# Performance work log

Measured on AMD Instinct MI355X. Metric: run time of the kernel, lower is better.

## Reference

```python
import jax, jax.numpy as jnp
import numpy as np


def _make_pert(r, s):
    lin = np.linspace(-r, r, s)
    xm, ym, tm = np.meshgrid(lin, lin, lin)  # default 'xy' indexing, matches torch code
    return jnp.asarray(np.stack([xm.ravel(), ym.ravel(), tm.ravel()], axis=-1), dtype=jnp.float32)

PERTS = (_make_pert(0.01, 3), _make_pert(0.05, 5), _make_pert(0.09, 7))  # [27,3],[125,3],[343,3]

N, IN, H, HQ, FF, OUT = 4096, 3, 256, 64, 64, 3


def setup_inputs():
    key = jax.random.key(0)
    ks = jax.random.split(key, 24)

    def W(k, i, o):
        return (jax.random.normal(k, (i, o), jnp.float32) / np.sqrt(i)).astype(jnp.float32)

    one = jnp.ones((1,), jnp.float32)
    return {
        "x": jax.random.normal(ks[0], (N, 1), jnp.float32),
        "y": jax.random.normal(ks[1], (N, 1), jnp.float32),
        "t": jax.random.normal(ks[2], (N, 1), jnp.float32),
        # linear_emb: 3 -> 64 -> WaveAct -> 256
        "emb_W1": W(ks[3], IN, HQ), "emb_b1": jnp.zeros((HQ,), jnp.float32),
        "emb_wa": one, "emb_wb": one,
        "emb_W2": W(ks[4], HQ, H), "emb_b2": jnp.zeros((H,), jnp.float32),
        # multiregion_mixer: 4 -> 8 -> WaveAct -> 1
        "mix_W1": W(ks[5], 4, 8), "mix_b1": jnp.zeros((8,), jnp.float32),
        "mix_wa": one, "mix_wb": one,
        "mix_W2": W(ks[6], 8, 1), "mix_b2": jnp.zeros((1,), jnp.float32),
        "out_W0": W(ks[7], H, FF), "out_b0": jnp.zeros((FF,), jnp.float32),
        "out_wa0": one, "out_wb0": one,
        "out_Wh": jnp.stack([W(ks[8 + i], FF, FF) for i in range(3)]),
        "out_bh": jnp.zeros((3, FF), jnp.float32),
        "out_wah": jnp.ones((3, 1), jnp.float32), "out_wbh": jnp.ones((3, 1), jnp.float32),
        "out_Wf1": W(ks[11], FF, FF), "out_bf1": jnp.zeros((FF,), jnp.float32),
        "out_waf": one, "out_wbf": one,
        "out_Wf2": W(ks[12], FF, OUT), "out_bf2": jnp.zeros((OUT,), jnp.float32),
    }


def _wave(h, wa, wb):
    return wa * jnp.sin(h) + wb * jnp.cos(h)


def reference(x, y, t,
              emb_W1, emb_b1, emb_wa, emb_wb, emb_W2, emb_b2,
              mix_W1, mix_b1, mix_wa, mix_wb, mix_W2, mix_b2,
              out_W0, out_b0, out_wa0, out_wb0,
              out_Wh, out_bh, out_wah, out_wbh,
              out_Wf1, out_bf1, out_waf, out_wbf, out_Wf2, out_bf2):
    def emb(s):  # [..., 3] -> [..., 256]
        h = _wave(s @ emb_W1 + emb_b1, emb_wa, emb_wb)
        return h @ emb_W2 + emb_b2

    src = jnp.concatenate([x, y, t], axis=-1)           # [N, 3]
    feats = [emb(src)]                                   # region 1: unperturbed
    for P in PERTS:
        perturbed = src[:, None, :] + P[None, :, :]      # [N, P, 3]
        feats.append(emb(perturbed).mean(axis=1))        # [N, 256]
    stacked = jnp.stack(feats, axis=-1)                  # [N, 256, 4] (== permute(0,2,1) of stack dim=1)

    m = _wave(stacked @ mix_W1 + mix_b1, mix_wa, mix_wb) # [N, 256, 8]
    e = (m @ mix_W2 + mix_b2)[:, :, 0]                   # [N, 256]

    h = _wave(e @ out_W0 + out_b0, out_wa0, out_wb0)     # [N, 64]
    for i in range(3):                                   # fixed num_layer-1 = 3 hidden layers
        h = _wave(h @ out_Wh[i] + out_bh[i], out_wah[i], out_wbh[i])
    h = _wave(h @ out_Wf1 + out_bf1, out_waf, out_wbf)
    return h @ out_Wf2 + out_bf2                         # [N, 3]
```

## Files before the change

### kernel.cpp

```cpp
#include <hip/hip_runtime.h>

typedef _Float16 f16;
typedef _Float16 f16x8 __attribute__((ext_vector_type(8)));
typedef float v4f __attribute__((ext_vector_type(4)));

#define WS_W2T  0
#define WS_W0T  16384
#define WS_WHT  32768
#define WS_WF1T 45056
#define WS_CDW  24576

__global__ __launch_bounds__(256) void preprocess(
    const float* __restrict__ embW1, const float* __restrict__ embW2,
    const float* __restrict__ outW0, const float* __restrict__ outWh,
    const float* __restrict__ outWf1, f16* __restrict__ wsh)
{
    const int g = blockIdx.x * 256 + threadIdx.x;
    if (g < 16384) {
        const int c = g >> 6, k = g & 63;
        wsh[WS_W2T + g] = (f16)embW2[k*256 + c];
    } else if (g < 32768) {
        const int i = g - 16384;
        const int f = i >> 8, k = i & 255;
        wsh[WS_W0T + i] = (f16)outW0[k*64 + f];
    } else if (g < 45056) {
        const int i = g - 32768;
        const int l = i >> 12, f = (i >> 6) & 63, k = i & 63;
        wsh[WS_WHT + i] = (f16)outWh[l*4096 + k*64 + f];
    } else if (g < 49152) {
        const int i = g - 45056;
        const int f = i >> 6, k = i & 63;
        wsh[WS_WF1T + i] = (f16)outWf1[k*64 + f];
    } else if (g < 49344) {
        const int i = g - 49152;
        const int r = i >> 6, ch = i & 63;
        const float w0 = embW1[ch], w1 = embW1[64 + ch], w2 = embW1[128 + ch];
        float v;
        if (r == 0) {
            v = (1.f + 2.f*__cosf(0.01f*w0)) * (1.f + 2.f*__cosf(0.01f*w1))
              * (1.f + 2.f*__cosf(0.01f*w2)) * (1.f/27.f);
        } else if (r == 1) {
            v = (1.f + 2.f*(__cosf(0.025f*w0) + __cosf(0.05f*w0)))
              * (1.f + 2.f*(__cosf(0.025f*w1) + __cosf(0.05f*w1)))
              * (1.f + 2.f*(__cosf(0.025f*w2) + __cosf(0.05f*w2))) * (1.f/125.f);
        } else {
            v = (1.f + 2.f*(__cosf(0.03f*w0) + __cosf(0.06f*w0) + __cosf(0.09f*w0)))
              * (1.f + 2.f*(__cosf(0.03f*w1) + __cosf(0.06f*w1) + __cosf(0.09f*w1)))
              * (1.f + 2.f*(__cosf(0.03f*w2) + __cosf(0.06f*w2) + __cosf(0.09f*w2))) * (1.f/343.f);
        }
        ((float*)wsh)[WS_CDW + i] = v;
    }
}

__global__ __launch_bounds__(256) void model_mfma(
    const float* __restrict__ x, const float* __restrict__ y, const float* __restrict__ t,
    const float* __restrict__ embW1, const float* __restrict__ embb1,
    const float* __restrict__ embwa, const float* __restrict__ embwb,
    const float* __restrict__ embb2,
    const float* __restrict__ mixW1, const float* __restrict__ mixb1,
    const float* __restrict__ mixwa, const float* __restrict__ mixwb,
    const float* __restrict__ mixW2, const float* __restrict__ mixb2,
    const float* __restrict__ outb0,
    const float* __restrict__ outwa0, const float* __restrict__ outwb0,
    const float* __restrict__ outbh,
    const float* __restrict__ outwah, const float* __restrict__ outwbh,
    const float* __restrict__ outbf1,
    const float* __restrict__ outwaf, const float* __restrict__ outwbf,
    const float* __restrict__ outWf2, const float* __restrict__ outbf2,
    const f16* __restrict__ wsh,
    float* __restrict__ out, int N)
{
    __shared__ __attribute__((aligned(16))) f16 sW2T[256*72];
    __shared__ __attribute__((aligned(16))) f16 sA[64*72];
    __shared__ __attribute__((aligned(16))) f16 sE[16*264];
    __shared__ __attribute__((aligned(16))) f16 sH[2][16*72];
    __shared__ float sHf[16*65];

    const int tid  = threadIdx.x;
    const int lane = tid & 63;
    const int wv   = tid >> 6;
    const int n0   = blockIdx.x * 16;

    {
        const uint4* src = (const uint4*)(wsh + WS_W2T + tid*64);
        uint4* dst = (uint4*)(sW2T + tid*72);
        #pragma unroll
        for (int i = 0; i < 8; ++i) dst[i] = src[i];
    }

    {
        const int k = tid & 63;
        const int sq = tid >> 6;
        const float w0 = embW1[k], w1 = embW1[64+k], w2 = embW1[128+k];
        const float b1 = embb1[k];
        const float ewa = embwa[0], ewb = embwb[0];
        const float* Cw = (const float*)wsh + WS_CDW;
        const float c1 = Cw[k], c2 = Cw[64+k], c3 = Cw[128+k];
        #pragma unroll
        for (int q = 0; q < 4; ++q) {
            const int s = sq*4 + q;
            const int ns = (n0 + s < N) ? (n0 + s) : (N - 1);
            const float u = fmaf(x[ns], w0, fmaf(y[ns], w1, fmaf(t[ns], w2, b1)));
            const float sv = ewa*__sinf(u) + ewb*__cosf(u);
            f16* row = sA + (s*4)*72 + k;
            row[0]   = (f16)sv;
            row[72]  = (f16)(sv*c1);
            row[144] = (f16)(sv*c2);
            row[216] = (f16)(sv*c3);
        }
    }
    __syncthreads();

    const int l15 = lane & 15, qb = lane >> 4;

    {
        const f16x8 af0 = *(const f16x8*)(sA + (16*wv + l15)*72 + qb*8);
        const f16x8 af1 = *(const f16x8*)(sA + (16*wv + l15)*72 + 32 + qb*8);
        const int s_loc = 4*wv + qb;
        const float mwa = mixwa[0], mwb = mixwb[0], mb2v = mixb2[0];
        #pragma unroll
        for (int nt = 0; nt < 16; ++nt) {
            const f16x8 bf0 = *(const f16x8*)(sW2T + (16*nt + l15)*72 + qb*8);
            const f16x8 bf1 = *(const f16x8*)(sW2T + (16*nt + l15)*72 + 32 + qb*8);
            v4f acc = {0.f, 0.f, 0.f, 0.f};
            acc = __builtin_amdgcn_mfma_f32_16x16x32_f16(af0, bf0, acc, 0, 0, 0);
            acc = __builtin_amdgcn_mfma_f32_16x16x32_f16(af1, bf1, acc, 0, 0, 0);
            const int c = 16*nt + l15;
            const float b2c = embb2[c];
            const float s0 = acc[0]+b2c, s1 = acc[1]+b2c, s2 = acc[2]+b2c, s3 = acc[3]+b2c;
            float ev = mb2v;
            #pragma unroll
            for (int j = 0; j < 8; ++j) {
                float p = fmaf(s0, mixW1[j],
                          fmaf(s1, mixW1[8+j],
                          fmaf(s2, mixW1[16+j],
                          fmaf(s3, mixW1[24+j], mixb1[j]))));
                ev = fmaf(mwa*__sinf(p) + mwb*__cosf(p), mixW2[j], ev);
            }
            sE[s_loc*264 + c] = (f16)ev;
        }
    }
    __syncthreads();

    const int fme = 16*wv + l15;

    {
        v4f acc = {0.f, 0.f, 0.f, 0.f};
        const f16* Ae   = sE + l15*264 + qb*8;
        const f16* W0Tg = wsh + WS_W0T + fme*256 + qb*8;
        #pragma unroll
        for (int kt = 0; kt < 8; ++kt) {
            const f16x8 af = *(const f16x8*)(Ae + kt*32);
            const f16x8 bf = *(const f16x8*)(W0Tg + kt*32);
            acc = __builtin_amdgcn_mfma_f32_16x16x32_f16(af, bf, acc, 0, 0, 0);
        }
        const float b0 = outb0[fme], wa = outwa0[0], wb = outwb0[0];
        #pragma unroll
        for (int r = 0; r < 4; ++r) {
            const float a = acc[r] + b0;
            sH[0][(qb*4 + r)*72 + fme] = (f16)(wa*__sinf(a) + wb*__cosf(a));
        }
    }
    __syncthreads();

    int cur = 0;
    #pragma unroll
    for (int i = 0; i < 4; ++i) {
        const f16* Wg = (i < 3) ? (wsh + WS_WHT + i*4096) : (wsh + WS_WF1T);
        v4f acc = {0.f, 0.f, 0.f, 0.f};
        #pragma unroll
        for (int kt = 0; kt < 2; ++kt) {
            const f16x8 af = *(const f16x8*)(sH[cur] + l15*72 + kt*32 + qb*8);
            const f16x8 bf = *(const f16x8*)(Wg + fme*64 + kt*32 + qb*8);
            acc = __builtin_amdgcn_mfma_f32_16x16x32_f16(af, bf, acc, 0, 0, 0);
        }
        float bias, wa, wb;
        if (i < 3) { bias = outbh[i*64 + fme]; wa = outwah[i]; wb = outwbh[i]; }
        else       { bias = outbf1[fme];       wa = outwaf[0]; wb = outwbf[0]; }
        #pragma unroll
        for (int r = 0; r < 4; ++r) {
            const float a = acc[r] + bias;
            const float v = wa*__sinf(a) + wb*__cosf(a);
            if (i < 3) sH[cur^1][(qb*4 + r)*72 + fme] = (f16)v;
            else       sHf[(qb*4 + r)*65 + fme] = v;
        }
        __syncthreads();
        cur ^= 1;
    }

    if (tid < 48) {
        const int s = tid / 3, o = tid - s*3;
        float a = outbf2[o];
        #pragma unroll 16
        for (int k = 0; k < 64; ++k)
            a = fmaf(sHf[s*65 + k], outWf2[k*3 + o], a);
        const int gn = n0 + s;
        if (gn < N) out[gn*3 + o] = a;
    }
}

extern "C" void kernel_launch(void* const* d_in, const int* in_sizes, int n_in,
                              void* d_out, int out_size, void* d_ws, size_t ws_size,
                              hipStream_t stream) {
    const float* x      = (const float*)d_in[0];
    const float* y      = (const float*)d_in[1];
    const float* t      = (const float*)d_in[2];
    const float* embW1  = (const float*)d_in[3];
    const float* embb1  = (const float*)d_in[4];
    const float* embwa  = (const float*)d_in[5];
    const float* embwb  = (const float*)d_in[6];
    const float* embW2  = (const float*)d_in[7];
    const float* embb2  = (const float*)d_in[8];
    const float* mixW1  = (const float*)d_in[9];
    const float* mixb1  = (const float*)d_in[10];
    const float* mixwa  = (const float*)d_in[11];
    const float* mixwb  = (const float*)d_in[12];
    const float* mixW2  = (const float*)d_in[13];
    const float* mixb2  = (const float*)d_in[14];
    const float* outW0  = (const float*)d_in[15];
    const float* outb0  = (const float*)d_in[16];
    const float* outwa0 = (const float*)d_in[17];
    const float* outwb0 = (const float*)d_in[18];
    const float* outWh  = (const float*)d_in[19];
    const float* outbh  = (const float*)d_in[20];
    const float* outwah = (const float*)d_in[21];
    const float* outwbh = (const float*)d_in[22];
    const float* outWf1 = (const float*)d_in[23];
    const float* outbf1 = (const float*)d_in[24];
    const float* outwaf = (const float*)d_in[25];
    const float* outwbf = (const float*)d_in[26];
    const float* outWf2 = (const float*)d_in[27];
    const float* outbf2 = (const float*)d_in[28];
    float* out = (float*)d_out;
    f16* wsh = (f16*)d_ws;

    const int N = in_sizes[0];

    preprocess<<<193, 256, 0, stream>>>(embW1, embW2, outW0, outWh, outWf1, wsh);

    const int blocks = (N + 15) / 16;
    model_mfma<<<blocks, 256, 0, stream>>>(
        x, y, t,
        embW1, embb1, embwa, embwb, embb2,
        mixW1, mixb1, mixwa, mixwb, mixW2, mixb2,
        outb0, outwa0, outwb0,
        outbh, outwah, outwbh,
        outbf1, outwaf, outwbf, outWf2, outbf2,
        wsh, out, N);
}
```

Baseline: 126.2 us.

## Shrink blocks to four samples, read W2 from global, fold WaveAct into phase-shifted sine

```diff
diff --git a/kernel.cpp b/kernel.cpp
--- a/kernel.cpp
+++ b/kernel.cpp
@@ -9,11 +9,18 @@
 #define WS_WHT  32768
 #define WS_WF1T 45056
 #define WS_CDW  24576
+#define WS_RPHI 24768
 
 __global__ __launch_bounds__(256) void preprocess(
     const float* __restrict__ embW1, const float* __restrict__ embW2,
     const float* __restrict__ outW0, const float* __restrict__ outWh,
-    const float* __restrict__ outWf1, f16* __restrict__ wsh)
+    const float* __restrict__ outWf1,
+    const float* __restrict__ embwa, const float* __restrict__ embwb,
+    const float* __restrict__ mixwa, const float* __restrict__ mixwb,
+    const float* __restrict__ outwa0, const float* __restrict__ outwb0,
+    const float* __restrict__ outwah, const float* __restrict__ outwbh,
+    const float* __restrict__ outwaf, const float* __restrict__ outwbf,
+    f16* __restrict__ wsh)
 {
     const int g = blockIdx.x * 256 + threadIdx.x;
     if (g < 16384) {
@@ -49,83 +56,77 @@
               * (1.f + 2.f*(__cosf(0.03f*w2) + __cosf(0.06f*w2) + __cosf(0.09f*w2))) * (1.f/343.f);
         }
         ((float*)wsh)[WS_CDW + i] = v;
+    } else if (g < 49360) {
+        const int i = g - 49344;
+        const int p = i >> 1;
+        float wa, wb;
+        switch (p) {
+            case 0: wa = embwa[0];  wb = embwb[0];  break;
+            case 1: wa = mixwa[0];  wb = mixwb[0];  break;
+            case 2: wa = outwa0[0]; wb = outwb0[0]; break;
+            case 3: case 4: case 5: wa = outwah[p-3]; wb = outwbh[p-3]; break;
+            default: wa = outwaf[0]; wb = outwbf[0]; break;
+        }
+        const float v = (i & 1) ? atan2f(wb, wa) : sqrtf(wa*wa + wb*wb);
+        ((float*)wsh)[WS_RPHI + p*2 + (i & 1)] = v;
     }
 }
 
-__global__ __launch_bounds__(256) void model_mfma(
+__global__ __launch_bounds__(256, 4) void model_mfma(
     const float* __restrict__ x, const float* __restrict__ y, const float* __restrict__ t,
     const float* __restrict__ embW1, const float* __restrict__ embb1,
-    const float* __restrict__ embwa, const float* __restrict__ embwb,
     const float* __restrict__ embb2,
     const float* __restrict__ mixW1, const float* __restrict__ mixb1,
-    const float* __restrict__ mixwa, const float* __restrict__ mixwb,
     const float* __restrict__ mixW2, const float* __restrict__ mixb2,
-    const float* __restrict__ outb0,
-    const float* __restrict__ outwa0, const float* __restrict__ outwb0,
-    const float* __restrict__ outbh,
-    const float* __restrict__ outwah, const float* __restrict__ outwbh,
+    const float* __restrict__ outb0, const float* __restrict__ outbh,
     const float* __restrict__ outbf1,
-    const float* __restrict__ outwaf, const float* __restrict__ outwbf,
     const float* __restrict__ outWf2, const float* __restrict__ outbf2,
     const f16* __restrict__ wsh,
     float* __restrict__ out, int N)
 {
-    __shared__ __attribute__((aligned(16))) f16 sW2T[256*72];
-    __shared__ __attribute__((aligned(16))) f16 sA[64*72];
+    __shared__ __attribute__((aligned(16))) f16 sA[16*72];
     __shared__ __attribute__((aligned(16))) f16 sE[16*264];
     __shared__ __attribute__((aligned(16))) f16 sH[2][16*72];
-    __shared__ float sHf[16*65];
+    __shared__ float sHf[4*65];
 
     const int tid  = threadIdx.x;
     const int lane = tid & 63;
     const int wv   = tid >> 6;
-    const int n0   = blockIdx.x * 16;
+    const int n0   = blockIdx.x * 4;
+    const float* rphi = (const float*)wsh + WS_RPHI;
 
     {
-        const uint4* src = (const uint4*)(wsh + WS_W2T + tid*64);
-        uint4* dst = (uint4*)(sW2T + tid*72);
-        #pragma unroll
-        for (int i = 0; i < 8; ++i) dst[i] = src[i];
-    }
-
-    {
-        const int k = tid & 63;
-        const int sq = tid >> 6;
+        const int k = lane, sq = wv;
         const float w0 = embW1[k], w1 = embW1[64+k], w2 = embW1[128+k];
         const float b1 = embb1[k];
-        const float ewa = embwa[0], ewb = embwb[0];
         const float* Cw = (const float*)wsh + WS_CDW;
         const float c1 = Cw[k], c2 = Cw[64+k], c3 = Cw[128+k];
+        const int ns = (n0 + sq < N) ? (n0 + sq) : (N - 1);
+        const float u = fmaf(x[ns], w0, fmaf(y[ns], w1, fmaf(t[ns], w2, b1)));
+        const float sv = rphi[0] * __sinf(u + rphi[1]);
+        f16* row = sA + (sq*4)*72 + k;
+        row[0]   = (f16)sv;
+        row[72]  = (f16)(sv*c1);
+        row[144] = (f16)(sv*c2);
+        row[216] = (f16)(sv*c3);
+    }
+    __syncthreads();
+
+    const int l15 = lane & 15, qb = lane >> 4;
+
+    {
+        const f16x8 af0 = *(const f16x8*)(sA + l15*72 + qb*8);
+        const f16x8 af1 = *(const f16x8*)(sA + l15*72 + 32 + qb*8);
+        const float mR = rphi[2], mP = rphi[3], mb2v = mixb2[0];
         #pragma unroll
-        for (int q = 0; q < 4; ++q) {
-            const int s = sq*4 + q;
-            const int ns = (n0 + s < N) ? (n0 + s) : (N - 1);
-            const float u = fmaf(x[ns], w0, fmaf(y[ns], w1, fmaf(t[ns], w2, b1)));
-            const float sv = ewa*__sinf(u) + ewb*__cosf(u);
-            f16* row = sA + (s*4)*72 + k;
-            row[0]   = (f16)sv;
-            row[72]  = (f16)(sv*c1);
-            row[144] = (f16)(sv*c2);
-            row[216] = (f16)(sv*c3);
-        }
-    }
-    __syncthreads();
-
-    const int l15 = lane & 15, qb = lane >> 4;
-
-    {
-        const f16x8 af0 = *(const f16x8*)(sA + (16*wv + l15)*72 + qb*8);
-        const f16x8 af1 = *(const f16x8*)(sA + (16*wv + l15)*72 + 32 + qb*8);
-        const int s_loc = 4*wv + qb;
-        const float mwa = mixwa[0], mwb = mixwb[0], mb2v = mixb2[0];
-        #pragma unroll
-        for (int nt = 0; nt < 16; ++nt) {
-            const f16x8 bf0 = *(const f16x8*)(sW2T + (16*nt + l15)*72 + qb*8);
-            const f16x8 bf1 = *(const f16x8*)(sW2T + (16*nt + l15)*72 + 32 + qb*8);
+        for (int nt = 0; nt < 4; ++nt) {
+            const int cb = wv*64 + nt*16;
+            const f16x8 bf0 = *(const f16x8*)(wsh + WS_W2T + (cb + l15)*64 + qb*8);
+            const f16x8 bf1 = *(const f16x8*)(wsh + WS_W2T + (cb + l15)*64 + 32 + qb*8);
             v4f acc = {0.f, 0.f, 0.f, 0.f};
             acc = __builtin_amdgcn_mfma_f32_16x16x32_f16(af0, bf0, acc, 0, 0, 0);
             acc = __builtin_amdgcn_mfma_f32_16x16x32_f16(af1, bf1, acc, 0, 0, 0);
-            const int c = 16*nt + l15;
+            const int c = cb + l15;
             const float b2c = embb2[c];
             const float s0 = acc[0]+b2c, s1 = acc[1]+b2c, s2 = acc[2]+b2c, s3 = acc[3]+b2c;
             float ev = mb2v;
@@ -135,14 +136,14 @@
                           fmaf(s1, mixW1[8+j],
                           fmaf(s2, mixW1[16+j],
                           fmaf(s3, mixW1[24+j], mixb1[j]))));
-                ev = fmaf(mwa*__sinf(p) + mwb*__cosf(p), mixW2[j], ev);
+                ev = fmaf(mR*__sinf(p + mP), mixW2[j], ev);
             }
-            sE[s_loc*264 + c] = (f16)ev;
+            sE[qb*264 + c] = (f16)ev;
         }
     }
     __syncthreads();
 
-    const int fme = 16*wv + l15;
+    const int fme = wv*16 + l15;
 
     {
         v4f acc = {0.f, 0.f, 0.f, 0.f};
@@ -154,11 +155,11 @@
             const f16x8 bf = *(const f16x8*)(W0Tg + kt*32);
             acc = __builtin_amdgcn_mfma_f32_16x16x32_f16(af, bf, acc, 0, 0, 0);
         }
-        const float b0 = outb0[fme], wa = outwa0[0], wb = outwb0[0];
-        #pragma unroll
-        for (int r = 0; r < 4; ++r) {
-            const float a = acc[r] + b0;
-            sH[0][(qb*4 + r)*72 + fme] = (f16)(wa*__sinf(a) + wb*__cosf(a));
+        if (qb == 0) {
+            const float b0 = outb0[fme], R = rphi[4], P = rphi[5];
+            #pragma unroll
+            for (int r = 0; r < 4; ++r)
+                sH[0][r*72 + fme] = (f16)(R*__sinf(acc[r] + b0 + P));
         }
     }
     __syncthreads();
@@ -174,21 +175,22 @@
             const f16x8 bf = *(const f16x8*)(Wg + fme*64 + kt*32 + qb*8);
             acc = __builtin_amdgcn_mfma_f32_16x16x32_f16(af, bf, acc, 0, 0, 0);
         }
-        float bias, wa, wb;
-        if (i < 3) { bias = outbh[i*64 + fme]; wa = outwah[i]; wb = outwbh[i]; }
-        else       { bias = outbf1[fme];       wa = outwaf[0]; wb = outwbf[0]; }
-        #pragma unroll
-        for (int r = 0; r < 4; ++r) {
-            const float a = acc[r] + bias;
-            const float v = wa*__sinf(a) + wb*__cosf(a);
-            if (i < 3) sH[cur^1][(qb*4 + r)*72 + fme] = (f16)v;
-            else       sHf[(qb*4 + r)*65 + fme] = v;
+        if (qb == 0) {
+            float bias, R, P;
+            if (i < 3) { bias = outbh[i*64 + fme]; R = rphi[6+2*i]; P = rphi[7+2*i]; }
+            else       { bias = outbf1[fme];       R = rphi[12];    P = rphi[13]; }
+            #pragma unroll
+            for (int r = 0; r < 4; ++r) {
+                const float v = R*__sinf(acc[r] + bias + P);
+                if (i < 3) sH[cur^1][r*72 + fme] = (f16)v;
+                else       sHf[r*65 + fme] = v;
+            }
         }
         __syncthreads();
         cur ^= 1;
     }
 
-    if (tid < 48) {
+    if (tid < 12) {
         const int s = tid / 3, o = tid - s*3;
         float a = outbf2[o];
         #pragma unroll 16
@@ -236,15 +238,16 @@
 
     const int N = in_sizes[0];
 
-    preprocess<<<193, 256, 0, stream>>>(embW1, embW2, outW0, outWh, outWf1, wsh);
-
-    const int blocks = (N + 15) / 16;
+    preprocess<<<193, 256, 0, stream>>>(embW1, embW2, outW0, outWh, outWf1,
+                                        embwa, embwb, mixwa, mixwb,
+                                        outwa0, outwb0, outwah, outwbh,
+                                        outwaf, outwbf, wsh);
+
+    const int blocks = (N + 3) / 4;
     model_mfma<<<blocks, 256, 0, stream>>>(
         x, y, t,
-        embW1, embb1, embwa, embwb, embb2,
-        mixW1, mixb1, mixwa, mixwb, mixW2, mixb2,
-        outb0, outwa0, outwb0,
-        outbh, outwah, outwbh,
-        outbf1, outwaf, outwbf, outWf2, outbf2,
+        embW1, embb1, embb2,
+        mixW1, mixb1, mixW2, mixb2,
+        outb0, outbh, outbf1, outWf2, outbf2,
         wsh, out, N);
 }
```

New measurement: 126.0 us. About the same (-0.2%).

## Drop weight-preprocess kernel and run one fused kernel with 4 samples per block

Applied to the files above, without the earlier changes.

```diff
diff --git a/kernel.cpp b/kernel.cpp
--- a/kernel.cpp
+++ b/kernel.cpp
@@ -4,128 +4,76 @@
 typedef _Float16 f16x8 __attribute__((ext_vector_type(8)));
 typedef float v4f __attribute__((ext_vector_type(4)));
 
-#define WS_W2T  0
-#define WS_W0T  16384
-#define WS_WHT  32768
-#define WS_WF1T 45056
-#define WS_CDW  24576
-
-__global__ __launch_bounds__(256) void preprocess(
-    const float* __restrict__ embW1, const float* __restrict__ embW2,
-    const float* __restrict__ outW0, const float* __restrict__ outWh,
-    const float* __restrict__ outWf1, f16* __restrict__ wsh)
-{
-    const int g = blockIdx.x * 256 + threadIdx.x;
-    if (g < 16384) {
-        const int c = g >> 6, k = g & 63;
-        wsh[WS_W2T + g] = (f16)embW2[k*256 + c];
-    } else if (g < 32768) {
-        const int i = g - 16384;
-        const int f = i >> 8, k = i & 255;
-        wsh[WS_W0T + i] = (f16)outW0[k*64 + f];
-    } else if (g < 45056) {
-        const int i = g - 32768;
-        const int l = i >> 12, f = (i >> 6) & 63, k = i & 63;
-        wsh[WS_WHT + i] = (f16)outWh[l*4096 + k*64 + f];
-    } else if (g < 49152) {
-        const int i = g - 45056;
-        const int f = i >> 6, k = i & 63;
-        wsh[WS_WF1T + i] = (f16)outWf1[k*64 + f];
-    } else if (g < 49344) {
-        const int i = g - 49152;
-        const int r = i >> 6, ch = i & 63;
-        const float w0 = embW1[ch], w1 = embW1[64 + ch], w2 = embW1[128 + ch];
-        float v;
-        if (r == 0) {
-            v = (1.f + 2.f*__cosf(0.01f*w0)) * (1.f + 2.f*__cosf(0.01f*w1))
-              * (1.f + 2.f*__cosf(0.01f*w2)) * (1.f/27.f);
-        } else if (r == 1) {
-            v = (1.f + 2.f*(__cosf(0.025f*w0) + __cosf(0.05f*w0)))
-              * (1.f + 2.f*(__cosf(0.025f*w1) + __cosf(0.05f*w1)))
-              * (1.f + 2.f*(__cosf(0.025f*w2) + __cosf(0.05f*w2))) * (1.f/125.f);
-        } else {
-            v = (1.f + 2.f*(__cosf(0.03f*w0) + __cosf(0.06f*w0) + __cosf(0.09f*w0)))
-              * (1.f + 2.f*(__cosf(0.03f*w1) + __cosf(0.06f*w1) + __cosf(0.09f*w1)))
-              * (1.f + 2.f*(__cosf(0.03f*w2) + __cosf(0.06f*w2) + __cosf(0.09f*w2))) * (1.f/343.f);
-        }
-        ((float*)wsh)[WS_CDW + i] = v;
-    }
-}
-
-__global__ __launch_bounds__(256) void model_mfma(
+__global__ __launch_bounds__(256, 4) void model_one(
     const float* __restrict__ x, const float* __restrict__ y, const float* __restrict__ t,
     const float* __restrict__ embW1, const float* __restrict__ embb1,
     const float* __restrict__ embwa, const float* __restrict__ embwb,
-    const float* __restrict__ embb2,
+    const float* __restrict__ embW2, const float* __restrict__ embb2,
     const float* __restrict__ mixW1, const float* __restrict__ mixb1,
     const float* __restrict__ mixwa, const float* __restrict__ mixwb,
     const float* __restrict__ mixW2, const float* __restrict__ mixb2,
-    const float* __restrict__ outb0,
+    const float* __restrict__ outW0, const float* __restrict__ outb0,
     const float* __restrict__ outwa0, const float* __restrict__ outwb0,
-    const float* __restrict__ outbh,
+    const float* __restrict__ outWh, const float* __restrict__ outbh,
     const float* __restrict__ outwah, const float* __restrict__ outwbh,
-    const float* __restrict__ outbf1,
+    const float* __restrict__ outWf1, const float* __restrict__ outbf1,
     const float* __restrict__ outwaf, const float* __restrict__ outwbf,
     const float* __restrict__ outWf2, const float* __restrict__ outbf2,
-    const f16* __restrict__ wsh,
     float* __restrict__ out, int N)
 {
-    __shared__ __attribute__((aligned(16))) f16 sW2T[256*72];
-    __shared__ __attribute__((aligned(16))) f16 sA[64*72];
+    __shared__ __attribute__((aligned(16))) f16 sA[16*72];
     __shared__ __attribute__((aligned(16))) f16 sE[16*264];
     __shared__ __attribute__((aligned(16))) f16 sH[2][16*72];
-    __shared__ float sHf[16*65];
+    __shared__ float sHf[4*65];
 
     const int tid  = threadIdx.x;
     const int lane = tid & 63;
     const int wv   = tid >> 6;
-    const int n0   = blockIdx.x * 16;
+    const int n0   = blockIdx.x * 4;
 
     {
-        const uint4* src = (const uint4*)(wsh + WS_W2T + tid*64);
-        uint4* dst = (uint4*)(sW2T + tid*72);
-        #pragma unroll
-        for (int i = 0; i < 8; ++i) dst[i] = src[i];
-    }
-
-    {
-        const int k = tid & 63;
-        const int sq = tid >> 6;
+        const int k = lane;
         const float w0 = embW1[k], w1 = embW1[64+k], w2 = embW1[128+k];
         const float b1 = embb1[k];
-        const float ewa = embwa[0], ewb = embwb[0];
-        const float* Cw = (const float*)wsh + WS_CDW;
-        const float c1 = Cw[k], c2 = Cw[64+k], c3 = Cw[128+k];
-        #pragma unroll
-        for (int q = 0; q < 4; ++q) {
-            const int s = sq*4 + q;
-            const int ns = (n0 + s < N) ? (n0 + s) : (N - 1);
-            const float u = fmaf(x[ns], w0, fmaf(y[ns], w1, fmaf(t[ns], w2, b1)));
-            const float sv = ewa*__sinf(u) + ewb*__cosf(u);
-            f16* row = sA + (s*4)*72 + k;
-            row[0]   = (f16)sv;
-            row[72]  = (f16)(sv*c1);
-            row[144] = (f16)(sv*c2);
-            row[216] = (f16)(sv*c3);
-        }
+        const float ga = (1.f + 2.f*__cosf(0.01f*w0))
+                       * (1.f + 2.f*__cosf(0.01f*w1))
+                       * (1.f + 2.f*__cosf(0.01f*w2)) * (1.f/27.f);
+        const float gb = (1.f + 2.f*(__cosf(0.025f*w0) + __cosf(0.05f*w0)))
+                       * (1.f + 2.f*(__cosf(0.025f*w1) + __cosf(0.05f*w1)))
+                       * (1.f + 2.f*(__cosf(0.025f*w2) + __cosf(0.05f*w2))) * (1.f/125.f);
+        const float gc = (1.f + 2.f*(__cosf(0.03f*w0) + __cosf(0.06f*w0) + __cosf(0.09f*w0)))
+                       * (1.f + 2.f*(__cosf(0.03f*w1) + __cosf(0.06f*w1) + __cosf(0.09f*w1)))
+                       * (1.f + 2.f*(__cosf(0.03f*w2) + __cosf(0.06f*w2) + __cosf(0.09f*w2))) * (1.f/343.f);
+        const int ns = (n0 + wv < N) ? (n0 + wv) : (N - 1);
+        const float u = fmaf(x[ns], w0, fmaf(y[ns], w1, fmaf(t[ns], w2, b1)));
+        const float sv = embwa[0]*__sinf(u) + embwb[0]*__cosf(u);
+        f16* row = sA + (wv*4)*72 + k;
+        row[0]   = (f16)sv;
+        row[72]  = (f16)(sv*ga);
+        row[144] = (f16)(sv*gb);
+        row[216] = (f16)(sv*gc);
     }
     __syncthreads();
 
     const int l15 = lane & 15, qb = lane >> 4;
 
     {
-        const f16x8 af0 = *(const f16x8*)(sA + (16*wv + l15)*72 + qb*8);
-        const f16x8 af1 = *(const f16x8*)(sA + (16*wv + l15)*72 + 32 + qb*8);
-        const int s_loc = 4*wv + qb;
+        const f16x8 af0 = *(const f16x8*)(sA + l15*72 + qb*8);
+        const f16x8 af1 = *(const f16x8*)(sA + l15*72 + 32 + qb*8);
         const float mwa = mixwa[0], mwb = mixwb[0], mb2v = mixb2[0];
         #pragma unroll
-        for (int nt = 0; nt < 16; ++nt) {
-            const f16x8 bf0 = *(const f16x8*)(sW2T + (16*nt + l15)*72 + qb*8);
-            const f16x8 bf1 = *(const f16x8*)(sW2T + (16*nt + l15)*72 + 32 + qb*8);
+        for (int nt = 0; nt < 4; ++nt) {
+            const int c = wv*64 + nt*16 + l15;
+            const float* Wp = embW2 + (qb*8)*256 + c;
+            f16x8 bf0, bf1;
+            #pragma unroll
+            for (int j = 0; j < 8; ++j) {
+                bf0[j] = (f16)Wp[j*256];
+                bf1[j] = (f16)Wp[j*256 + 8192];
+            }
             v4f acc = {0.f, 0.f, 0.f, 0.f};
             acc = __builtin_amdgcn_mfma_f32_16x16x32_f16(af0, bf0, acc, 0, 0, 0);
             acc = __builtin_amdgcn_mfma_f32_16x16x32_f16(af1, bf1, acc, 0, 0, 0);
-            const int c = 16*nt + l15;
             const float b2c = embb2[c];
             const float s0 = acc[0]+b2c, s1 = acc[1]+b2c, s2 = acc[2]+b2c, s3 = acc[3]+b2c;
             float ev = mb2v;
@@ -137,28 +85,32 @@
                           fmaf(s3, mixW1[24+j], mixb1[j]))));
                 ev = fmaf(mwa*__sinf(p) + mwb*__cosf(p), mixW2[j], ev);
             }
-            sE[s_loc*264 + c] = (f16)ev;
+            sE[qb*264 + c] = (f16)ev;
         }
     }
     __syncthreads();
 
-    const int fme = 16*wv + l15;
+    const int fme = wv*16 + l15;
 
     {
         v4f acc = {0.f, 0.f, 0.f, 0.f};
-        const f16* Ae   = sE + l15*264 + qb*8;
-        const f16* W0Tg = wsh + WS_W0T + fme*256 + qb*8;
+        const f16* Ae = sE + l15*264 + qb*8;
         #pragma unroll
         for (int kt = 0; kt < 8; ++kt) {
             const f16x8 af = *(const f16x8*)(Ae + kt*32);
-            const f16x8 bf = *(const f16x8*)(W0Tg + kt*32);
+            const float* Wp = outW0 + (kt*32 + qb*8)*64 + fme;
+            f16x8 bf;
+            #pragma unroll
+            for (int j = 0; j < 8; ++j) bf[j] = (f16)Wp[j*64];
             acc = __builtin_amdgcn_mfma_f32_16x16x32_f16(af, bf, acc, 0, 0, 0);
         }
-        const float b0 = outb0[fme], wa = outwa0[0], wb = outwb0[0];
-        #pragma unroll
-        for (int r = 0; r < 4; ++r) {
-            const float a = acc[r] + b0;
-            sH[0][(qb*4 + r)*72 + fme] = (f16)(wa*__sinf(a) + wb*__cosf(a));
+        if (qb == 0) {
+            const float b0 = outb0[fme], wa = outwa0[0], wb = outwb0[0];
+            #pragma unroll
+            for (int r = 0; r < 4; ++r) {
+                const float a = acc[r] + b0;
+                sH[0][r*72 + fme] = (f16)(wa*__sinf(a) + wb*__cosf(a));
+            }
         }
     }
     __syncthreads();
@@ -166,29 +118,34 @@
     int cur = 0;
     #pragma unroll
     for (int i = 0; i < 4; ++i) {
-        const f16* Wg = (i < 3) ? (wsh + WS_WHT + i*4096) : (wsh + WS_WF1T);
+        const float* Wg = (i < 3) ? (outWh + i*4096) : outWf1;
         v4f acc = {0.f, 0.f, 0.f, 0.f};
         #pragma unroll
         for (int kt = 0; kt < 2; ++kt) {
             const f16x8 af = *(const f16x8*)(sH[cur] + l15*72 + kt*32 + qb*8);
-            const f16x8 bf = *(const f16x8*)(Wg + fme*64 + kt*32 + qb*8);
+            const float* Wp = Wg + (kt*32 + qb*8)*64 + fme;
+            f16x8 bf;
+            #pragma unroll
+            for (int j = 0; j < 8; ++j) bf[j] = (f16)Wp[j*64];
             acc = __builtin_amdgcn_mfma_f32_16x16x32_f16(af, bf, acc, 0, 0, 0);
         }
-        float bias, wa, wb;
-        if (i < 3) { bias = outbh[i*64 + fme]; wa = outwah[i]; wb = outwbh[i]; }
-        else       { bias = outbf1[fme];       wa = outwaf[0]; wb = outwbf[0]; }
-        #pragma unroll
-        for (int r = 0; r < 4; ++r) {
-            const float a = acc[r] + bias;
-            const float v = wa*__sinf(a) + wb*__cosf(a);
-            if (i < 3) sH[cur^1][(qb*4 + r)*72 + fme] = (f16)v;
-            else       sHf[(qb*4 + r)*65 + fme] = v;
+        if (qb == 0) {
+            float bias, wa, wb;
+            if (i < 3) { bias = outbh[i*64 + fme]; wa = outwah[i]; wb = outwbh[i]; }
+            else       { bias = outbf1[fme];       wa = outwaf[0]; wb = outwbf[0]; }
+            #pragma unroll
+            for (int r = 0; r < 4; ++r) {
+                const float a = acc[r] + bias;
+                const float v = wa*__sinf(a) + wb*__cosf(a);
+                if (i < 3) sH[cur^1][r*72 + fme] = (f16)v;
+                else       sHf[r*65 + fme] = v;
+            }
         }
         __syncthreads();
         cur ^= 1;
     }
 
-    if (tid < 48) {
+    if (tid < 12) {
         const int s = tid / 3, o = tid - s*3;
         float a = outbf2[o];
         #pragma unroll 16
@@ -232,19 +189,15 @@
     const float* outWf2 = (const float*)d_in[27];
     const float* outbf2 = (const float*)d_in[28];
     float* out = (float*)d_out;
-    f16* wsh = (f16*)d_ws;
 
     const int N = in_sizes[0];
-
-    preprocess<<<193, 256, 0, stream>>>(embW1, embW2, outW0, outWh, outWf1, wsh);
-
-    const int blocks = (N + 15) / 16;
-    model_mfma<<<blocks, 256, 0, stream>>>(
+    const int blocks = (N + 3) / 4;
+    model_one<<<blocks, 256, 0, stream>>>(
         x, y, t,
-        embW1, embb1, embwa, embwb, embb2,
+        embW1, embb1, embwa, embwb, embW2, embb2,
         mixW1, mixb1, mixwa, mixwb, mixW2, mixb2,
-        outb0, outwa0, outwb0,
-        outbh, outwah, outwbh,
-        outbf1, outwaf, outwbf, outWf2, outbf2,
-        wsh, out, N);
+        outW0, outb0, outwa0, outwb0,
+        outWh, outbh, outwah, outwbh,
+        outWf1, outbf1, outwaf, outwbf, outWf2, outbf2,
+        out, N);
 }
```

Result: no change. 126.1 us (-0.1%).
